# Kernel tuning notes

Hardware: AMD Instinct MI355X
Metric: run time of the kernel (lower is better)

The kernel has to match this reference:

```python
import jax, jax.numpy as jnp
import numpy as np

WIN_H = WIN_W = 7
NUM_HEADS = 6
DIM = 192
HEAD_DIM = DIM // NUM_HEADS
NUM_WIN = 1024
B_ = 8192
N = WIN_H * WIN_W


def _relative_position_index(win_h, win_w):
    coords = np.stack(np.meshgrid(np.arange(win_h), np.arange(win_w), indexing='ij'))  # (2,h,w)
    flat = coords.reshape(2, -1)
    rel = flat[:, :, None] - flat[:, None, :]          # (2, N, N)
    rel = rel.transpose(1, 2, 0).astype(np.int32)      # (N, N, 2)
    rel[:, :, 0] += win_h - 1
    rel[:, :, 1] += win_w - 1
    rel[:, :, 0] *= 2 * win_w - 1
    return rel.sum(-1)                                 # (N, N) in [0, (2h-1)(2w-1))


def setup_inputs() -> dict:
    key = jax.random.key(0)
    ks = jax.random.split(key, 7)
    return {
        'x': jax.random.normal(ks[0], (B_, N, DIM), jnp.float32),
        'mask': jax.random.normal(ks[1], (NUM_WIN, N, N), jnp.float32),
        'qkv_w': jax.random.normal(ks[2], (3 * DIM, DIM), jnp.float32) * 0.02,
        'qkv_b': jax.random.normal(ks[3], (3 * DIM,), jnp.float32) * 0.02,
        'proj_w': jax.random.normal(ks[4], (DIM, DIM), jnp.float32) * 0.02,
        'proj_b': jax.random.normal(ks[5], (DIM,), jnp.float32) * 0.02,
        'rpb_table': jax.random.normal(ks[6], ((2 * WIN_H - 1) * (2 * WIN_W - 1), NUM_HEADS), jnp.float32) * 0.02,
        'rel_index': jnp.asarray(_relative_position_index(WIN_H, WIN_W)),
    }


def reference(x, mask, qkv_w, qkv_b, proj_w, proj_b, rpb_table, rel_index):
    B, n, C = x.shape
    H, hd = NUM_HEADS, HEAD_DIM
    scale = hd ** (-0.5)

    qkv = (x @ qkv_w.T + qkv_b).reshape(B, n, 3, H, hd)
    qkv = jnp.transpose(qkv, (2, 0, 3, 1, 4))          # (3, B, H, N, hd)
    q, k, v = qkv[0], qkv[1], qkv[2]

    attn = jnp.einsum('bhnd,bhmd->bhnm', q * scale, k)  # (B, H, N, N)

    # gathered relative position bias: (N*N,) -> (N, N, H) -> (H, N, N)
    bias = rpb_table[rel_index.reshape(-1)].reshape(n, n, H)
    attn = attn + jnp.transpose(bias, (2, 0, 1))[None]

    num_win = mask.shape[0]
    attn = attn.reshape(B // num_win, num_win, H, n, n) + mask[None, :, None]
    attn = jax.nn.softmax(attn, axis=-1).reshape(B, H, n, n)

    out = jnp.einsum('bhnm,bhmd->bhnd', attn, v)         # (B, H, N, hd)
    out = jnp.transpose(out, (0, 2, 1, 3)).reshape(B, n, H * hd)
    return out @ proj_w.T + proj_b
```

## Files before the change

### kernel.cpp

```cpp
#include <hip/hip_runtime.h>

#define NTOK  49
#define NWIN  1024
#define SCALE 0.17677669529663687f

#define SMEM_BYTES 77824

typedef __bf16 bfx8 __attribute__((ext_vector_type(8)));
typedef float  f32x4 __attribute__((ext_vector_type(4)));
typedef unsigned long long ull;

union BF8 { bfx8 v; ull q[2]; };

__device__ __forceinline__ unsigned short f2bf(float f) {
    unsigned int u = __builtin_bit_cast(unsigned int, f);
    u += 0x7fffu + ((u >> 16) & 1u);
    return (unsigned short)(u >> 16);
}
__device__ __forceinline__ ull pack4(f32x4 a) {
    return (ull)f2bf(a[0]) | ((ull)f2bf(a[1]) << 16) |
           ((ull)f2bf(a[2]) << 32) | ((ull)f2bf(a[3]) << 48);
}

extern "C" __global__ void wattn_prep(const float* __restrict__ qkv_w,
                                      const float* __restrict__ proj_w,
                                      const float* __restrict__ rpb,
                                      const int*   __restrict__ rel,
                                      const float* __restrict__ qkv_b,
                                      unsigned short* __restrict__ W1f,
                                      unsigned short* __restrict__ W2p,
                                      float* __restrict__ qkvbs,
                                      float* __restrict__ biasT)
{
    const int i = blockIdx.x * 256 + threadIdx.x;
    if (i < 110592) {
        const int e = i & 7, l = (i >> 3) & 63, f = i >> 9;
        const int kk = f % 6, oct = f / 6;
        const int R = oct * 16 + (l & 15), C = kk * 32 + (l >> 4) * 8 + e;
        float v = qkv_w[R * 192 + C];
        if (oct < 12) v *= SCALE;
        W1f[i] = f2bf(v);
    }
    if (i < 36864) {
        const int e = i & 7, l = (i >> 3) & 63, f = i >> 9;
        const int c2t = f / 6, H = f % 6;
        const int R = c2t * 16 + (l & 15);
        const int C = H * 32 + (e >> 2) * 16 + (l >> 4) * 4 + (e & 3);
        W2p[i] = f2bf(proj_w[R * 192 + C]);
    }
    if (i < 576) qkvbs[i] = (i < 192) ? qkv_b[i] * SCALE : qkv_b[i];
    if (i < 6 * NTOK * 64) {
        const int h = i / (NTOK * 64), j = (i / 64) % NTOK, ii = i % 64;
        biasT[i] = (ii < NTOK) ? rpb[rel[ii * NTOK + j] * 6 + h] : 0.f;
    }
}

extern "C" __global__ void __launch_bounds__(512, 2)
wattn_fused(const float* __restrict__ x,
            const float* __restrict__ mask,
            const float* __restrict__ proj_b,
            const unsigned short* __restrict__ W1f,
            const unsigned short* __restrict__ W2p,
            const float* __restrict__ qkvbs,
            const float* __restrict__ biasT,
            float* __restrict__ out)
{
    __shared__ char smem[SMEM_BYTES];
    char* const XB  = smem;
    char* const OBX = smem;
    char* const KBp = smem + 25600;
    char* const VTp = smem + 50176;

    const int tid  = threadIdx.x;
    const int wave = tid >> 6;
    const int lane = tid & 63;
    const int g    = lane >> 4;
    const int jn   = lane & 15;
    const int qt   = wave & 3;
    const int hh   = wave >> 2;
    const size_t b = blockIdx.x;

#pragma unroll
    for (int u = 0; u < 3; ++u) {
        const int i = tid + u * 512;
        if (i < 1500)
            *(unsigned int*)(XB + (49 + i / 100) * 400 + (i % 100) * 4) = 0u;
    }
    {
        const float4* xw = (const float4*)(x + b * 9408);
#pragma unroll
        for (int u = 0; u < 5; ++u) {
            const int i = tid + u * 512;
            if (i < 2352) {
                float4 v = xw[i];
                *(ull*)(XB + (i / 48) * 400 + (i % 48) * 8) =
                    (ull)f2bf(v.x) | ((ull)f2bf(v.y) << 16) |
                    ((ull)f2bf(v.z) << 32) | ((ull)f2bf(v.w) << 48);
            }
        }
    }
    __syncthreads();

    BF8 qf[3];
    {
        bfx8 xq[6];
#pragma unroll
        for (int kk = 0; kk < 6; ++kk)
            xq[kk] = *(const bfx8*)(XB + (qt * 16 + jn) * 400 + kk * 64 + g * 16);
#pragma unroll
        for (int qp = 0; qp < 3; ++qp) {
            ull lo, hi;
#pragma unroll
            for (int s = 0; s < 2; ++s) {
                const int oct = hh * 6 + qp * 2 + s;
                f32x4 acc = *(const f32x4*)(qkvbs + oct * 16 + 4 * g);
#pragma unroll
                for (int kk = 0; kk < 6; ++kk) {
                    bfx8 wq = *(const bfx8*)(W1f + ((size_t)(oct * 6 + kk) * 64 + lane) * 8);
                    acc = __builtin_amdgcn_mfma_f32_16x16x32_bf16(wq, xq[kk], acc, 0, 0, 0);
                }
                if (s == 0) lo = pack4(acc); else hi = pack4(acc);
            }
            qf[qp].q[0] = lo; qf[qp].q[1] = hi;
        }
    }

#pragma unroll
    for (int oo = 0; oo < 3; ++oo) {
        const int oct = (hh ? 24 : 12) + qt * 3 + oo;
        const int ct12 = qt * 3 + oo;
        bfx8 af[6];
#pragma unroll
        for (int kk = 0; kk < 6; ++kk)
            af[kk] = *(const bfx8*)(W1f + ((size_t)(oct * 6 + kk) * 64 + lane) * 8);
        const f32x4 binitK = *(const f32x4*)(qkvbs + oct * 16 + 4 * g);
        const float bv = qkvbs[oct * 16 + jn];
#pragma unroll
        for (int tt = 0; tt < 4; ++tt) {
            bfx8 xf[6];
#pragma unroll
            for (int kk = 0; kk < 6; ++kk)
                xf[kk] = *(const bfx8*)(XB + (tt * 16 + jn) * 400 + kk * 64 + g * 16);
            if (!hh) {
                f32x4 acc = binitK;
#pragma unroll
                for (int kk = 0; kk < 6; ++kk)
                    acc = __builtin_amdgcn_mfma_f32_16x16x32_bf16(af[kk], xf[kk], acc, 0, 0, 0);
                *(ull*)(KBp + ((tt * 6 + (ct12 >> 1)) * 64 + lane) * 16 + (ct12 & 1) * 8) = pack4(acc);
            } else {
                f32x4 acc = {bv, bv, bv, bv};
#pragma unroll
                for (int kk = 0; kk < 6; ++kk)
                    acc = __builtin_amdgcn_mfma_f32_16x16x32_bf16(xf[kk], af[kk], acc, 0, 0, 0);
                *(ull*)(VTp + (ct12 * 16 + jn) * 144 + (tt >> 1) * 64 + g * 16 + (tt & 1) * 8) = pack4(acc);
            }
        }
    }
    __syncthreads();

    const int iq = qt * 16 + jn;
    const int ic = iq < NTOK ? iq : NTOK - 1;
    const float* mw = mask + (b & (NWIN - 1)) * (NTOK * NTOK);
    float mv[4][4];
#pragma unroll
    for (int kt = 0; kt < 4; ++kt)
#pragma unroll
        for (int r = 0; r < 4; ++r) {
            const int j = kt * 16 + 4 * g + r;
            const int jc = j < NTOK ? j : NTOK - 1;
            mv[kt][r] = mw[ic * NTOK + jc];
        }

    BF8 obf[3];
#pragma unroll
    for (int hl = 0; hl < 3; ++hl) {
        const int H = hh * 3 + hl;
        f32x4 s[4];
#pragma unroll
        for (int kt = 0; kt < 4; ++kt) {
            bfx8 kf = *(const bfx8*)(KBp + ((kt * 6 + H) * 64 + lane) * 16);
            f32x4 z = {0.f, 0.f, 0.f, 0.f};
            s[kt] = __builtin_amdgcn_mfma_f32_16x16x32_bf16(kf, qf[hl].v, z, 0, 0, 0);
        }
        f32x4 p[4];
        float mx = -1e30f;
#pragma unroll
        for (int kt = 0; kt < 4; ++kt)
#pragma unroll
            for (int r = 0; r < 4; ++r) {
                const int j = kt * 16 + 4 * g + r;
                const int jc = j < NTOK ? j : NTOK - 1;
                const float bmv = biasT[((size_t)H * NTOK + jc) * 64 + iq];
                const float v = (j < NTOK) ? s[kt][r] + bmv + mv[kt][r] : -1e30f;
                p[kt][r] = v;
                mx = fmaxf(mx, v);
            }
        mx = fmaxf(mx, __shfl_xor(mx, 16));
        mx = fmaxf(mx, __shfl_xor(mx, 32));
        float sum = 0.f;
#pragma unroll
        for (int kt = 0; kt < 4; ++kt)
#pragma unroll
            for (int r = 0; r < 4; ++r) {
                p[kt][r] = __expf(p[kt][r] - mx);
                sum += p[kt][r];
            }
        sum += __shfl_xor(sum, 16);
        sum += __shfl_xor(sum, 32);
        const float inv = 1.f / sum;
        BF8 p01, p23;
        p01.q[0] = pack4(p[0]); p01.q[1] = pack4(p[1]);
        p23.q[0] = pack4(p[2]); p23.q[1] = pack4(p[3]);
#pragma unroll
        for (int ct = 0; ct < 2; ++ct) {
            const int row = H * 32 + ct * 16 + jn;
            bfx8 v0 = *(const bfx8*)(VTp + row * 144 + g * 16);
            bfx8 v1 = *(const bfx8*)(VTp + row * 144 + 64 + g * 16);
            f32x4 o = {0.f, 0.f, 0.f, 0.f};
            o = __builtin_amdgcn_mfma_f32_16x16x32_bf16(v0, p01.v, o, 0, 0, 0);
            o = __builtin_amdgcn_mfma_f32_16x16x32_bf16(v1, p23.v, o, 0, 0, 0);
            obf[hl].q[ct] = pack4(o * inv);
        }
    }
    __syncthreads();

#pragma unroll
    for (int hl = 0; hl < 3; ++hl)
        *(bfx8*)(OBX + (((hh * 4 + qt) * 3 + hl) * 64 + lane) * 16) = obf[hl].v;
    __syncthreads();

    const int oh = 1 - hh;
    float* outp = out + b * 9408;
#pragma unroll
    for (int c6 = 0; c6 < 6; ++c6) {
        const int c2t = hh * 6 + c6;
        f32x4 acc = *(const f32x4*)(proj_b + c2t * 16 + 4 * g);
#pragma unroll
        for (int hl = 0; hl < 3; ++hl) {
            bfx8 wfa = *(const bfx8*)(W2p + ((size_t)(c2t * 6 + hh * 3 + hl) * 64 + lane) * 8);
            acc = __builtin_amdgcn_mfma_f32_16x16x32_bf16(wfa, obf[hl].v, acc, 0, 0, 0);
            bfx8 wfb = *(const bfx8*)(W2p + ((size_t)(c2t * 6 + oh * 3 + hl) * 64 + lane) * 8);
            bfx8 ob2 = *(const bfx8*)(OBX + (((oh * 4 + qt) * 3 + hl) * 64 + lane) * 16);
            acc = __builtin_amdgcn_mfma_f32_16x16x32_bf16(wfb, ob2, acc, 0, 0, 0);
        }
        if (iq < NTOK)
            *(f32x4*)(outp + iq * 192 + c2t * 16 + 4 * g) = acc;
    }
}

extern "C" void kernel_launch(void* const* d_in, const int* in_sizes, int n_in,
                              void* d_out, int out_size, void* d_ws, size_t ws_size,
                              hipStream_t stream) {
    const float* x      = (const float*)d_in[0];
    const float* mask   = (const float*)d_in[1];
    const float* qkv_w  = (const float*)d_in[2];
    const float* qkv_b  = (const float*)d_in[3];
    const float* proj_w = (const float*)d_in[4];
    const float* proj_b = (const float*)d_in[5];
    const float* rpb    = (const float*)d_in[6];
    const int*   rel    = (const int*)d_in[7];
    float* outp = (float*)d_out;

    char* ws = (char*)d_ws;
    unsigned short* W1f = (unsigned short*)ws;
    unsigned short* W2p = (unsigned short*)(ws + 221184);
    float* qkvbs        = (float*)(ws + 221184 + 73728);
    float* biasT        = (float*)(ws + 221184 + 73728 + 2304);

    wattn_prep<<<432, 256, 0, stream>>>(qkv_w, proj_w, rpb, rel, qkv_b,
                                        W1f, W2p, qkvbs, biasT);
    wattn_fused<<<8192, 512, 0, stream>>>(x, mask, proj_b,
                                          W1f, W2p, qkvbs, biasT, outp);
}
```

Measured before the change: 512.9 us.

## Stage Q and attention output in LDS and redistribute projection GEMMs across waves

Q is now computed into shared memory, with all 36 QKV output tiles handed out round-robin across waves instead of each wave recomputing its own Q slice in registers. The output projection is split by output column tile over waves, each wave looping over all token tiles and heads from LDS. The relative-position bias table is transposed so each lane reads four biases with one vector load. The cost is that LDS grows from 76 KB to 100 KB, which may stop two blocks from sharing a CU. The round-robin split also leaves uneven work per wave: 36 tiles over 8 waves in QKV and 12 column tiles over 8 waves in the projection.

```diff
diff --git a/kernel.cpp b/kernel.cpp
--- a/kernel.cpp
+++ b/kernel.cpp
@@ -4,7 +4,7 @@
 #define NWIN  1024
 #define SCALE 0.17677669529663687f
 
-#define SMEM_BYTES 77824
+#define SMEM_BYTES 102400
 
 typedef __bf16 bfx8 __attribute__((ext_vector_type(8)));
 typedef float  f32x4 __attribute__((ext_vector_type(4)));
@@ -30,7 +30,7 @@
                                       unsigned short* __restrict__ W1f,
                                       unsigned short* __restrict__ W2p,
                                       float* __restrict__ qkvbs,
-                                      float* __restrict__ biasT)
+                                      float* __restrict__ biasN)
 {
     const int i = blockIdx.x * 256 + threadIdx.x;
     if (i < 110592) {
@@ -50,8 +50,8 @@
     }
     if (i < 576) qkvbs[i] = (i < 192) ? qkv_b[i] * SCALE : qkv_b[i];
     if (i < 6 * NTOK * 64) {
-        const int h = i / (NTOK * 64), j = (i / 64) % NTOK, ii = i % 64;
-        biasT[i] = (ii < NTOK) ? rpb[rel[ii * NTOK + j] * 6 + h] : 0.f;
+        const int h = i / (NTOK * 64), ii = (i / 64) % NTOK, j = i % 64;
+        biasN[i] = (j < NTOK) ? rpb[rel[ii * NTOK + j] * 6 + h] : 0.f;
     }
 }
 
@@ -62,14 +62,15 @@
             const unsigned short* __restrict__ W1f,
             const unsigned short* __restrict__ W2p,
             const float* __restrict__ qkvbs,
-            const float* __restrict__ biasT,
+            const float* __restrict__ biasN,
             float* __restrict__ out)
 {
     __shared__ char smem[SMEM_BYTES];
     char* const XB  = smem;
     char* const OBX = smem;
-    char* const KBp = smem + 25600;
-    char* const VTp = smem + 50176;
+    char* const QBp = smem + 25600;
+    char* const KBp = smem + 50176;
+    char* const VTp = smem + 74752;
 
     const int tid  = threadIdx.x;
     const int wave = tid >> 6;
@@ -101,57 +102,36 @@
     }
     __syncthreads();
 
-    BF8 qf[3];
-    {
-        bfx8 xq[6];
+    for (int oct = wave; oct < 36; oct += 8) {
+        bfx8 wf_[6];
 #pragma unroll
         for (int kk = 0; kk < 6; ++kk)
-            xq[kk] = *(const bfx8*)(XB + (qt * 16 + jn) * 400 + kk * 64 + g * 16);
-#pragma unroll
-        for (int qp = 0; qp < 3; ++qp) {
-            ull lo, hi;
-#pragma unroll
-            for (int s = 0; s < 2; ++s) {
-                const int oct = hh * 6 + qp * 2 + s;
-                f32x4 acc = *(const f32x4*)(qkvbs + oct * 16 + 4 * g);
+            wf_[kk] = *(const bfx8*)(W1f + ((size_t)(oct * 6 + kk) * 64 + lane) * 8);
+        if (oct < 24) {
+            const f32x4 binit = *(const f32x4*)(qkvbs + oct * 16 + 4 * g);
+            char* const dst = (oct < 12) ? QBp : KBp;
+            const int ct12 = (oct < 12) ? oct : oct - 12;
+#pragma unroll
+            for (int tt = 0; tt < 4; ++tt) {
+                f32x4 acc = binit;
 #pragma unroll
                 for (int kk = 0; kk < 6; ++kk) {
-                    bfx8 wq = *(const bfx8*)(W1f + ((size_t)(oct * 6 + kk) * 64 + lane) * 8);
-                    acc = __builtin_amdgcn_mfma_f32_16x16x32_bf16(wq, xq[kk], acc, 0, 0, 0);
+                    bfx8 xf = *(const bfx8*)(XB + (tt * 16 + jn) * 400 + kk * 64 + g * 16);
+                    acc = __builtin_amdgcn_mfma_f32_16x16x32_bf16(wf_[kk], xf, acc, 0, 0, 0);
                 }
-                if (s == 0) lo = pack4(acc); else hi = pack4(acc);
-            }
-            qf[qp].q[0] = lo; qf[qp].q[1] = hi;
-        }
-    }
-
-#pragma unroll
-    for (int oo = 0; oo < 3; ++oo) {
-        const int oct = (hh ? 24 : 12) + qt * 3 + oo;
-        const int ct12 = qt * 3 + oo;
-        bfx8 af[6];
-#pragma unroll
-        for (int kk = 0; kk < 6; ++kk)
-            af[kk] = *(const bfx8*)(W1f + ((size_t)(oct * 6 + kk) * 64 + lane) * 8);
-        const f32x4 binitK = *(const f32x4*)(qkvbs + oct * 16 + 4 * g);
-        const float bv = qkvbs[oct * 16 + jn];
-#pragma unroll
-        for (int tt = 0; tt < 4; ++tt) {
-            bfx8 xf[6];
-#pragma unroll
-            for (int kk = 0; kk < 6; ++kk)
-                xf[kk] = *(const bfx8*)(XB + (tt * 16 + jn) * 400 + kk * 64 + g * 16);
-            if (!hh) {
-                f32x4 acc = binitK;
-#pragma unroll
-                for (int kk = 0; kk < 6; ++kk)
-                    acc = __builtin_amdgcn_mfma_f32_16x16x32_bf16(af[kk], xf[kk], acc, 0, 0, 0);
-                *(ull*)(KBp + ((tt * 6 + (ct12 >> 1)) * 64 + lane) * 16 + (ct12 & 1) * 8) = pack4(acc);
-            } else {
+                *(ull*)(dst + ((tt * 6 + (ct12 >> 1)) * 64 + lane) * 16 + (ct12 & 1) * 8) = pack4(acc);
+            }
+        } else {
+            const float bv = qkvbs[oct * 16 + jn];
+            const int ct12 = oct - 24;
+#pragma unroll
+            for (int tt = 0; tt < 4; ++tt) {
                 f32x4 acc = {bv, bv, bv, bv};
 #pragma unroll
-                for (int kk = 0; kk < 6; ++kk)
-                    acc = __builtin_amdgcn_mfma_f32_16x16x32_bf16(xf[kk], af[kk], acc, 0, 0, 0);
+                for (int kk = 0; kk < 6; ++kk) {
+                    bfx8 xf = *(const bfx8*)(XB + (tt * 16 + jn) * 400 + kk * 64 + g * 16);
+                    acc = __builtin_amdgcn_mfma_f32_16x16x32_bf16(xf, wf_[kk], acc, 0, 0, 0);
+                }
                 *(ull*)(VTp + (ct12 * 16 + jn) * 144 + (tt >> 1) * 64 + g * 16 + (tt & 1) * 8) = pack4(acc);
             }
         }
@@ -171,30 +151,29 @@
             mv[kt][r] = mw[ic * NTOK + jc];
         }
 
-    BF8 obf[3];
 #pragma unroll
     for (int hl = 0; hl < 3; ++hl) {
         const int H = hh * 3 + hl;
-        f32x4 s[4];
+        bfx8 qfr = *(const bfx8*)(QBp + ((qt * 6 + H) * 64 + lane) * 16);
+        f32x4 p[4];
 #pragma unroll
         for (int kt = 0; kt < 4; ++kt) {
             bfx8 kf = *(const bfx8*)(KBp + ((kt * 6 + H) * 64 + lane) * 16);
             f32x4 z = {0.f, 0.f, 0.f, 0.f};
-            s[kt] = __builtin_amdgcn_mfma_f32_16x16x32_bf16(kf, qf[hl].v, z, 0, 0, 0);
-        }
-        f32x4 p[4];
+            p[kt] = __builtin_amdgcn_mfma_f32_16x16x32_bf16(kf, qfr, z, 0, 0, 0);
+        }
         float mx = -1e30f;
 #pragma unroll
-        for (int kt = 0; kt < 4; ++kt)
+        for (int kt = 0; kt < 4; ++kt) {
+            const f32x4 bm4 = *(const f32x4*)(biasN + ((size_t)H * NTOK + ic) * 64 + kt * 16 + 4 * g);
 #pragma unroll
             for (int r = 0; r < 4; ++r) {
                 const int j = kt * 16 + 4 * g + r;
-                const int jc = j < NTOK ? j : NTOK - 1;
-                const float bmv = biasT[((size_t)H * NTOK + jc) * 64 + iq];
-                const float v = (j < NTOK) ? s[kt][r] + bmv + mv[kt][r] : -1e30f;
+                const float v = (j < NTOK) ? p[kt][r] + bm4[r] + mv[kt][r] : -1e30f;
                 p[kt][r] = v;
                 mx = fmaxf(mx, v);
             }
+        }
         mx = fmaxf(mx, __shfl_xor(mx, 16));
         mx = fmaxf(mx, __shfl_xor(mx, 32));
         float sum = 0.f;
@@ -219,32 +198,30 @@
             f32x4 o = {0.f, 0.f, 0.f, 0.f};
             o = __builtin_amdgcn_mfma_f32_16x16x32_bf16(v0, p01.v, o, 0, 0, 0);
             o = __builtin_amdgcn_mfma_f32_16x16x32_bf16(v1, p23.v, o, 0, 0, 0);
-            obf[hl].q[ct] = pack4(o * inv);
+            *(ull*)(OBX + ((qt * 6 + H) * 64 + lane) * 16 + ct * 8) = pack4(o * inv);
         }
     }
     __syncthreads();
 
-#pragma unroll
-    for (int hl = 0; hl < 3; ++hl)
-        *(bfx8*)(OBX + (((hh * 4 + qt) * 3 + hl) * 64 + lane) * 16) = obf[hl].v;
-    __syncthreads();
-
-    const int oh = 1 - hh;
     float* outp = out + b * 9408;
-#pragma unroll
-    for (int c6 = 0; c6 < 6; ++c6) {
-        const int c2t = hh * 6 + c6;
-        f32x4 acc = *(const f32x4*)(proj_b + c2t * 16 + 4 * g);
-#pragma unroll
-        for (int hl = 0; hl < 3; ++hl) {
-            bfx8 wfa = *(const bfx8*)(W2p + ((size_t)(c2t * 6 + hh * 3 + hl) * 64 + lane) * 8);
-            acc = __builtin_amdgcn_mfma_f32_16x16x32_bf16(wfa, obf[hl].v, acc, 0, 0, 0);
-            bfx8 wfb = *(const bfx8*)(W2p + ((size_t)(c2t * 6 + oh * 3 + hl) * 64 + lane) * 8);
-            bfx8 ob2 = *(const bfx8*)(OBX + (((oh * 4 + qt) * 3 + hl) * 64 + lane) * 16);
-            acc = __builtin_amdgcn_mfma_f32_16x16x32_bf16(wfb, ob2, acc, 0, 0, 0);
-        }
-        if (iq < NTOK)
-            *(f32x4*)(outp + iq * 192 + c2t * 16 + 4 * g) = acc;
+    for (int c2t = wave; c2t < 12; c2t += 8) {
+        bfx8 wf2[6];
+#pragma unroll
+        for (int H = 0; H < 6; ++H)
+            wf2[H] = *(const bfx8*)(W2p + ((size_t)(c2t * 6 + H) * 64 + lane) * 8);
+        const f32x4 pb = *(const f32x4*)(proj_b + c2t * 16 + 4 * g);
+#pragma unroll
+        for (int qt2 = 0; qt2 < 4; ++qt2) {
+            f32x4 acc = pb;
+#pragma unroll
+            for (int H = 0; H < 6; ++H) {
+                bfx8 ob = *(const bfx8*)(OBX + ((qt2 * 6 + H) * 64 + lane) * 16);
+                acc = __builtin_amdgcn_mfma_f32_16x16x32_bf16(wf2[H], ob, acc, 0, 0, 0);
+            }
+            const int tok = qt2 * 16 + jn;
+            if (tok < NTOK)
+                *(f32x4*)(outp + tok * 192 + c2t * 16 + 4 * g) = acc;
+        }
     }
 }
 
@@ -265,10 +242,10 @@
     unsigned short* W1f = (unsigned short*)ws;
     unsigned short* W2p = (unsigned short*)(ws + 221184);
     float* qkvbs        = (float*)(ws + 221184 + 73728);
-    float* biasT        = (float*)(ws + 221184 + 73728 + 2304);
+    float* biasN        = (float*)(ws + 221184 + 73728 + 2304);
 
     wattn_prep<<<432, 256, 0, stream>>>(qkv_w, proj_w, rpb, rel, qkv_b,
-                                        W1f, W2p, qkvbs, biasT);
+                                        W1f, W2p, qkvbs, biasN);
     wattn_fused<<<8192, 512, 0, stream>>>(x, mask, proj_b,
-                                          W1f, W2p, qkvbs, biasT, outp);
-}
+                                          W1f, W2p, qkvbs, biasN, outp);
+}
```

Result: faster. 456.5 us (-11.0%).
